# Kernel optimization log

Hardware: AMD Instinct MI355X
Metric: run time of the kernel (lower is better)

Reference implementation:

```python
import jax, jax.numpy as jnp
import numpy as np

N_HEAD = 16

def setup_inputs() -> dict:
    key = jax.random.key(0)
    ks = jax.random.split(key, 9)
    B, T, C = 4, 2048, 1024
    s = 0.02
    return {
        "x": jax.random.normal(ks[0], (B, T, C), dtype=jnp.float32),
        "Wq": jax.random.normal(ks[1], (C, C), dtype=jnp.float32) * s,
        "bq": jnp.zeros((C,), dtype=jnp.float32),
        "Wk": jax.random.normal(ks[2], (C, C), dtype=jnp.float32) * s,
        "bk": jnp.zeros((C,), dtype=jnp.float32),
        "Wv": jax.random.normal(ks[3], (C, C), dtype=jnp.float32) * s,
        "bv": jnp.zeros((C,), dtype=jnp.float32),
        "Wo": jax.random.normal(ks[4], (C, C), dtype=jnp.float32) * s,
        "bo": jnp.zeros((C,), dtype=jnp.float32),
    }

def reference(x, Wq, bq, Wk, bk, Wv, bv, Wo, bo):
    B, T, C = x.shape
    H = N_HEAD
    d = C // H
    # QKV projections (Linear: y = x @ W + b), split heads -> [B, H, T, d]
    def proj(W, b):
        return (x @ W + b).reshape(B, T, H, d).transpose(0, 2, 1, 3)
    q = proj(Wq, bq)
    k = proj(Wk, bk)
    v = proj(Wv, bv)
    scale = jnp.float32(d) ** -0.5
    scores = jnp.einsum("bhtd,bhsd->bhts", q, k) * scale  # [B,H,T,T]
    attn = jax.nn.softmax(scores, axis=-1)
    out = jnp.einsum("bhts,bhsd->bhtd", attn, v)  # [B,H,T,d]
    out = out.transpose(0, 2, 1, 3).reshape(B, T, C)
    return out @ Wo + bo
```

## Files before the change

kernel.cpp:

```cpp
#include <hip/hip_runtime.h>
#include <hip/hip_bf16.h>

typedef unsigned short u16;
typedef unsigned int   u32;

typedef __bf16 bf16x8 __attribute__((ext_vector_type(8)));
typedef float  f32x4  __attribute__((ext_vector_type(4)));

#define MFMA16(A, B, C) __builtin_amdgcn_mfma_f32_16x16x32_bf16(A, B, C, 0, 0, 0)

static __device__ __forceinline__ u16 f2bf(float f) {
  union { float f; u32 u; } v; v.f = f;
  u32 r = v.u + 0x7fffu + ((v.u >> 16) & 1u);
  return (u16)(r >> 16);
}

static __device__ __forceinline__ float exp2a(float x) {
  float r; asm("v_exp_f32 %0, %1" : "=v"(r) : "v"(x)); return r;
}
static __device__ __forceinline__ float max3f(float a, float b, float c) {
  float r; asm("v_max3_f32 %0, %1, %2, %3" : "=v"(r) : "v"(a), "v"(b), "v"(c)); return r;
}
static __device__ __forceinline__ u32 cvtpk(float lo, float hi) {
  u32 r; asm("v_cvt_pk_bf16_f32 %0, %1, %2" : "=v"(r) : "v"(lo), "v"(hi)); return r;
}

static __device__ __forceinline__ void async16(const void* g, void* l) {
  __builtin_amdgcn_global_load_lds((const __attribute__((address_space(1))) void*)g,
                                   (__attribute__((address_space(3))) void*)l, 16, 0, 0);
}

static __device__ __forceinline__ int permrow(int r) {
  return (r & 3) | (((r >> 3) & 1) << 2);
}

__global__ __launch_bounds__(256) void cvtx_k(const float* __restrict__ x, u16* __restrict__ xb) {
  size_t i = ((size_t)blockIdx.x * 256 + threadIdx.x) * 4;
  float4 v = *(const float4*)(x + i);
  u32 lo = (u32)f2bf(v.x) | ((u32)f2bf(v.y) << 16);
  u32 hi = (u32)f2bf(v.z) | ((u32)f2bf(v.w) << 16);
  *(uint2*)(xb + i) = make_uint2(lo, hi);
}

__global__ __launch_bounds__(256) void wt_k(const float* __restrict__ Wq, const float* __restrict__ Wk,
                                            const float* __restrict__ Wv, const float* __restrict__ Wo,
                                            u16* __restrict__ WT) {
  const int z = blockIdx.z;
  const float* W = (z == 0) ? Wq : (z == 1) ? Wk : (z == 2) ? Wv : Wo;
  u16* out = WT + (size_t)z * 1048576;
  __shared__ float tile[32][33];
  const int tx = threadIdx.x & 31, ty = threadIdx.x >> 5;
  const int n0 = blockIdx.x * 32, k0 = blockIdx.y * 32;
#pragma unroll
  for (int i = 0; i < 4; i++)
    tile[ty + i * 8][tx] = W[(size_t)(k0 + ty + i * 8) * 1024 + n0 + tx];
  __syncthreads();
#pragma unroll
  for (int i = 0; i < 4; i++)
    out[(size_t)(n0 + ty + i * 8) * 1024 + k0 + tx] = f2bf(tile[tx][ty + i * 8]);
}

#define G_STAGE(NXT)                                                          \
  {                                                                           \
    async16(pgA0, &As[(NXT) * 16384 + (0 * 512 + tid) * 8]);                  \
    async16(pgA1, &As[(NXT) * 16384 + (1 * 512 + tid) * 8]);                  \
    async16(pgA2, &As[(NXT) * 16384 + (2 * 512 + tid) * 8]);                  \
    async16(pgA3, &As[(NXT) * 16384 + (3 * 512 + tid) * 8]);                  \
    async16(pgB0, &Bs[(NXT) * 8192 + (0 * 512 + tid) * 8]);                   \
    async16(pgB1, &Bs[(NXT) * 8192 + (1 * 512 + tid) * 8]);                   \
    pgA0 += 64; pgA1 += 64; pgA2 += 64; pgA3 += 64; pgB0 += 64; pgB1 += 64;   \
  }

#define COMPUTE_T(CUR)                                                        \
  _Pragma("unroll")                                                           \
  for (int kk = 0; kk < 2; ++kk) {                                            \
    const u16* pAk = kk ? pA1 : pA0;                                          \
    const u16* pBk = kk ? pB1 : pB0;                                          \
    bf16x8 a0 = *(const bf16x8*)(pAk + (CUR) * 16384);                        \
    bf16x8 a1 = *(const bf16x8*)(pAk + (CUR) * 16384 + 1024);                 \
    bf16x8 a2 = *(const bf16x8*)(pAk + (CUR) * 16384 + 2048);                 \
    bf16x8 a3 = *(const bf16x8*)(pAk + (CUR) * 16384 + 3072);                 \
    bf16x8 b0 = *(const bf16x8*)(pBk + (CUR) * 8192);                         \
    bf16x8 b1 = *(const bf16x8*)(pBk + (CUR) * 8192 + 1024);                  \
    bf16x8 b2 = *(const bf16x8*)(pBk + (CUR) * 8192 + 2048);                  \
    bf16x8 b3 = *(const bf16x8*)(pBk + (CUR) * 8192 + 3072);                  \
    __builtin_amdgcn_s_setprio(1);                                            \
    acc[0][0] = MFMA16(a0, b0, acc[0][0]); acc[0][1] = MFMA16(a0, b1, acc[0][1]); \
    acc[0][2] = MFMA16(a0, b2, acc[0][2]); acc[0][3] = MFMA16(a0, b3, acc[0][3]); \
    acc[1][0] = MFMA16(a1, b0, acc[1][0]); acc[1][1] = MFMA16(a1, b1, acc[1][1]); \
    acc[1][2] = MFMA16(a1, b2, acc[1][2]); acc[1][3] = MFMA16(a1, b3, acc[1][3]); \
    acc[2][0] = MFMA16(a2, b0, acc[2][0]); acc[2][1] = MFMA16(a2, b1, acc[2][1]); \
    acc[2][2] = MFMA16(a2, b2, acc[2][2]); acc[2][3] = MFMA16(a2, b3, acc[2][3]); \
    acc[3][0] = MFMA16(a3, b0, acc[3][0]); acc[3][1] = MFMA16(a3, b1, acc[3][1]); \
    acc[3][2] = MFMA16(a3, b2, acc[3][2]); acc[3][3] = MFMA16(a3, b3, acc[3][3]); \
    __builtin_amdgcn_s_setprio(0);                                            \
  }

#define GITER(CUR, WN, STG, NXT)                                              \
  {                                                                           \
    asm volatile("s_waitcnt vmcnt(" #WN ")" ::: "memory");                    \
    __builtin_amdgcn_s_barrier();                                             \
    __builtin_amdgcn_sched_barrier(0);                                        \
    if (STG) G_STAGE(NXT)                                                     \
    COMPUTE_T(CUR)                                                            \
  }

template <int MODE>
__global__ __launch_bounds__(512, 2) void gemm256_k(const u16* __restrict__ A, const u16* __restrict__ WTall,
                                                    const float* __restrict__ b0, const float* __restrict__ b1,
                                                    const float* __restrict__ b2,
                                                    u16* __restrict__ outb, float* __restrict__ outf) {
  __shared__ u16 As[3 * 16384];
  __shared__ u16 Bs[3 * 8192];
  const int tid = threadIdx.x;
  const int lane = tid & 63;
  const int wid = tid >> 6;
  const int wm = wid >> 1, wn = wid & 1;
  const int g = lane >> 4, cc = lane & 15;

  const int bid = blockIdx.x;
  const int xcd = bid & 7;
  const int idx = bid >> 3;
  const int m0 = (xcd * 4 + (idx & 3)) * 256;
  const int nb = (idx >> 2) * 128;
  const u16* Bg = WTall + (size_t)(MODE == 0 ? 0 : 3145728) + (size_t)nb * 1024;

  const u16* pgA0; const u16* pgA1; const u16* pgA2; const u16* pgA3;
  const u16* pgB0; const u16* pgB1;
  {
    const int u0 = tid, u1 = 512 + tid, u2 = 1024 + tid, u3 = 1536 + tid;
    pgA0 = A + (size_t)(m0 + (u0 >> 3)) * 1024 + (((u0 & 7) ^ ((u0 >> 3) & 7)) << 3);
    pgA1 = A + (size_t)(m0 + (u1 >> 3)) * 1024 + (((u1 & 7) ^ ((u1 >> 3) & 7)) << 3);
    pgA2 = A + (size_t)(m0 + (u2 >> 3)) * 1024 + (((u2 & 7) ^ ((u2 >> 3) & 7)) << 3);
    pgA3 = A + (size_t)(m0 + (u3 >> 3)) * 1024 + (((u3 & 7) ^ ((u3 >> 3) & 7)) << 3);
    pgB0 = Bg + (size_t)(u0 >> 3) * 1024 + (((u0 & 7) ^ ((u0 >> 3) & 7)) << 3);
    pgB1 = Bg + (size_t)(u1 >> 3) * 1024 + (((u1 & 7) ^ ((u1 >> 3) & 7)) << 3);
  }

  const int s0 = g ^ (cc & 7);
  const u16* pA0 = As + (wm * 64 + cc) * 64 + (s0 << 3);
  const u16* pA1 = As + (wm * 64 + cc) * 64 + ((s0 ^ 4) << 3);
  const u16* pB0 = Bs + (wn * 64 + cc) * 64 + (s0 << 3);
  const u16* pB1 = Bs + (wn * 64 + cc) * 64 + ((s0 ^ 4) << 3);

  f32x4 acc[4][4] = {};

  G_STAGE(0)
  G_STAGE(1)

  for (int to = 0; to < 12; to += 3) {
    GITER(0, 6, 1, 2)
    GITER(1, 6, 1, 0)
    GITER(2, 6, 1, 1)
  }
  GITER(0, 6, 1, 2)
  GITER(1, 6, 1, 0)
  GITER(2, 6, 0, 0)
  GITER(0, 0, 0, 0)

  const int z = (MODE == 0) ? (nb >> 10) : 0;
  const float* bias = (MODE == 0) ? (z == 0 ? b0 : (z == 1 ? b1 : b2)) : b0;
  const float scl = (MODE == 0 && z == 0) ? 0.18033688011112042f : 1.0f;

#pragma unroll
  for (int mi = 0; mi < 4; mi++) {
#pragma unroll
    for (int ni = 0; ni < 4; ni++) {
      const int ng = nb + wn * 64 + ni * 16 + cc;
      const int n = (MODE == 0) ? (ng & 1023) : ng;
      const float bn = bias[n];
      const int mb = m0 + wm * 64 + mi * 16 + g * 4;
      if (MODE == 0) {
        u16* o = outb + (size_t)z * 8388608;
        if (z == 2) {
          u16 h[4];
#pragma unroll
          for (int r = 0; r < 4; r++) h[r] = f2bf(acc[mi][ni][r] + bn);
          const size_t idx2 = ((size_t)(((mb >> 11) * 16 + (n >> 6)) * 64 + (n & 63))) * 2048 + (mb & 2047);
          *(uint2*)&o[idx2] = make_uint2((u32)h[0] | ((u32)h[1] << 16), (u32)h[2] | ((u32)h[3] << 16));
        } else {
#pragma unroll
          for (int r = 0; r < 4; r++) {
            const int m = mb + r;
            const float val = (acc[mi][ni][r] + bn) * scl;
            o[((size_t)((m >> 11) * 16 + (n >> 6)) * 2048 + (m & 2047)) * 64 + (n & 63)] = f2bf(val);
          }
        }
      } else {
#pragma unroll
        for (int r = 0; r < 4; r++)
          outf[(size_t)(mb + r) * 1024 + n] = acc[mi][ni][r] + bn;
      }
    }
  }
}

#define SMAX(S0, S1, M, O, PF)                                                \
  {                                                                           \
    float pm_ = max3f(max3f(S0[0], S0[1], S0[2]),                             \
                      max3f(S0[3], S1[0], S1[1]), fmaxf(S1[2], S1[3]));       \
    if (__builtin_expect(!__all(pm_ <= M + 8.0f), 0)) {                       \
      pm_ = fmaxf(pm_, __shfl_xor(pm_, 16));                                  \
      pm_ = fmaxf(pm_, __shfl_xor(pm_, 32));                                  \
      const float mn_ = fmaxf(M, pm_);                                        \
      const float al_ = exp2a(M - mn_);                                       \
      _Pragma("unroll")                                                       \
      for (int r_ = 0; r_ < 4; ++r_) {                                        \
        const float ar_ = __shfl(al_, g * 4 + r_);                            \
        _Pragma("unroll")                                                     \
        for (int t_ = 0; t_ < 5; ++t_) O[t_][r_] *= ar_;                      \
      }                                                                       \
      M = mn_;                                                                \
    }                                                                         \
    const float e0_ = exp2a(S0[0] - M), e1_ = exp2a(S0[1] - M);               \
    const float e2_ = exp2a(S0[2] - M), e3_ = exp2a(S0[3] - M);               \
    const float e4_ = exp2a(S1[0] - M), e5_ = exp2a(S1[1] - M);               \
    const float e6_ = exp2a(S1[2] - M), e7_ = exp2a(S1[3] - M);               \
    union { u32 u[4]; bf16x8 v; } pu_;                                        \
    pu_.u[0] = cvtpk(e0_, e1_); pu_.u[1] = cvtpk(e2_, e3_);                   \
    pu_.u[2] = cvtpk(e4_, e5_); pu_.u[3] = cvtpk(e6_, e7_);                   \
    PF = pu_.v;                                                               \
  }

#define COMPUTE(BUF)                                                          \
  _Pragma("unroll")                                                           \
  for (int sub = 0; sub < 2; ++sub) {                                         \
    const u16* pV_ = sub ? pV1 : pV0;                                         \
    bf16x8 k00 = *(const bf16x8*)(pK0 + (BUF)*4096 + sub*2048);               \
    bf16x8 k01 = *(const bf16x8*)(pK1 + (BUF)*4096 + sub*2048);               \
    bf16x8 k10 = *(const bf16x8*)(pK0 + (BUF)*4096 + sub*2048 + 256);         \
    bf16x8 k11 = *(const bf16x8*)(pK1 + (BUF)*4096 + sub*2048 + 256);         \
    __builtin_amdgcn_s_setprio(1);                                            \
    f32x4 sA0 = {}, sA1 = {}, sB0 = {}, sB1 = {};                             \
    sA0 = MFMA16(k00, qfA[0], sA0); sA0 = MFMA16(k01, qfA[1], sA0);           \
    sB0 = MFMA16(k00, qfB[0], sB0); sB0 = MFMA16(k01, qfB[1], sB0);           \
    sA1 = MFMA16(k10, qfA[0], sA1); sA1 = MFMA16(k11, qfA[1], sA1);           \
    sB1 = MFMA16(k10, qfB[0], sB1); sB1 = MFMA16(k11, qfB[1], sB1);           \
    __builtin_amdgcn_s_setprio(0);                                            \
    bf16x8 pfA, pfB;                                                          \
    SMAX(sA0, sA1, mA, oA, pfA);                                              \
    SMAX(sB0, sB1, mB, oB, pfB);                                              \
    __builtin_amdgcn_s_setprio(1);                                            \
    _Pragma("unroll")                                                         \
    for (int t = 0; t < 4; ++t) {                                             \
      bf16x8 vf = *(const bf16x8*)(pV_ + (BUF)*4096 + t*1024);                \
      oA[t] = MFMA16(pfA, vf, oA[t]);                                         \
      oB[t] = MFMA16(pfB, vf, oB[t]);                                         \
    }                                                                         \
    oA[4] = MFMA16(pfA, vone, oA[4]);                                         \
    oB[4] = MFMA16(pfB, vone, oB[4]);                                         \
    __builtin_amdgcn_s_setprio(0);                                            \
  }

#define STEP(BUF, IT)                                                         \
  {                                                                           \
    __syncthreads();                                                          \
    if ((IT) < 31) {                                                          \
      const size_t ko_ = (size_t)((IT) + 1) * 4096;                           \
      const size_t vo_ = (size_t)((IT) + 1) * 64;                             \
      async16(kS0 + ko_, &Ks[((BUF) ^ 1) * 4096 + tid * 8]);                  \
      async16(kS1 + ko_, &Ks[((BUF) ^ 1) * 4096 + tid * 8 + 2048]);           \
      async16(vS0 + vo_, &Vs[((BUF) ^ 1) * 4096 + tid * 8]);                  \
      async16(vS1 + vo_, &Vs[((BUF) ^ 1) * 4096 + tid * 8 + 2048]);           \
    }                                                                         \
    COMPUTE(BUF)                                                              \
  }

__global__ __launch_bounds__(256, 4) void attn_k(const u16* __restrict__ Qg, const u16* __restrict__ Kg,
                                                 const u16* __restrict__ Vtg, u16* __restrict__ ctx) {
  __shared__ u16 Ks[8192];
  __shared__ u16 Vs[8192];
  const int tid = threadIdx.x;
  const int lane = tid & 63;
  const int wid = tid >> 6;
  const int g = lane >> 4, cc = lane & 15;
  const int a_ = cc >> 2, b_ = cc & 3;

  const int bid = blockIdx.x;
  const int xcd = bid & 7, tt = bid >> 3;
  const int bh = xcd * 8 + (tt >> 4);
  const int q0 = (tt & 15) * 128 + wid * 16;
  const size_t base = (size_t)bh * 131072;

  bf16x8 qfA[2], qfB[2];
#pragma unroll
  for (int c2 = 0; c2 < 2; c2++) {
    qfA[c2] = *(const bf16x8*)(Qg + base + (size_t)(q0 + cc) * 64 + c2 * 32 + g * 8);
    qfB[c2] = *(const bf16x8*)(Qg + base + (size_t)(q0 + 64 + cc) * 64 + c2 * 32 + g * 8);
  }

  bf16x8 vone;
#pragma unroll
  for (int j = 0; j < 8; j++) vone[j] = (__bf16)1.0f;

  float mA = -30000.0f, mB = -30000.0f;
  f32x4 oA[5] = {}, oB[5] = {};

  const int cK = b_ | ((a_ & 1) << 2);
  const int slK = g ^ cK;
  const u16* pK0 = &Ks[(8 * a_ + b_) * 64 + (slK << 3)];
  const u16* pK1 = &Ks[(8 * a_ + b_) * 64 + ((slK ^ 4) << 3)];
  const int cV = b_ | (((cc >> 3) & 1) << 2);
  const u16* pV0 = &Vs[cc * 64 + ((g ^ cV) << 3)];
  const u16* pV1 = &Vs[cc * 64 + (((4 + g) ^ cV) << 3)];

  const int r0 = tid >> 3, r1 = r0 + 32;
  const int slot = tid & 7;
  const int sp0 = slot ^ permrow(r0), sp1 = slot ^ permrow(r1);
  const u16* kS0 = Kg + base + (size_t)r0 * 64 + (sp0 << 3);
  const u16* kS1 = Kg + base + (size_t)r1 * 64 + (sp1 << 3);
  const u16* vS0 = Vtg + base + (size_t)r0 * 2048 + (sp0 << 3);
  const u16* vS1 = Vtg + base + (size_t)r1 * 2048 + (sp1 << 3);

  async16(kS0, &Ks[tid * 8]);
  async16(kS1, &Ks[tid * 8 + 2048]);
  async16(vS0, &Vs[tid * 8]);
  async16(vS1, &Vs[tid * 8 + 2048]);

  for (int it = 0; it < 32; it += 2) {
    STEP(0, it)
    STEP(1, it + 1)
  }

  const int b = bh >> 4, h = bh & 15;
#pragma unroll
  for (int r = 0; r < 4; r++) {
    {
      const float inv = __builtin_amdgcn_rcpf(oA[4][r]);
      const int q = q0 + g * 4 + r;
#pragma unroll
      for (int t = 0; t < 4; t++)
        ctx[((size_t)((b * 2048 + q) * 16 + h)) * 64 + t * 16 + cc] = f2bf(oA[t][r] * inv);
    }
    {
      const float inv = __builtin_amdgcn_rcpf(oB[4][r]);
      const int q = q0 + 64 + g * 4 + r;
#pragma unroll
      for (int t = 0; t < 4; t++)
        ctx[((size_t)((b * 2048 + q) * 16 + h)) * 64 + t * 16 + cc] = f2bf(oB[t][r] * inv);
    }
  }
}

extern "C" void kernel_launch(void* const* d_in, const int* in_sizes, int n_in,
                              void* d_out, int out_size, void* d_ws, size_t ws_size,
                              hipStream_t stream) {
  const float* x  = (const float*)d_in[0];
  const float* Wq = (const float*)d_in[1];
  const float* bq = (const float*)d_in[2];
  const float* Wk = (const float*)d_in[3];
  const float* bk = (const float*)d_in[4];
  const float* Wv = (const float*)d_in[5];
  const float* bv = (const float*)d_in[6];
  const float* Wo = (const float*)d_in[7];
  const float* bo = (const float*)d_in[8];
  float* out = (float*)d_out;

  char* w = (char*)d_ws;
  u16* xb   = (u16*)(w);
  u16* WT   = (u16*)(w + (16u << 20));
  u16* QKV  = (u16*)(w + (24u << 20));
  u16* ctxb = (u16*)(w + (72u << 20));

  cvtx_k<<<dim3(8192), dim3(256), 0, stream>>>(x, xb);
  wt_k<<<dim3(32, 32, 4), dim3(256), 0, stream>>>(Wq, Wk, Wv, Wo, WT);
  gemm256_k<0><<<dim3(768), dim3(512), 0, stream>>>(xb, WT, bq, bk, bv, QKV, nullptr);
  attn_k<<<dim3(1024), dim3(256), 0, stream>>>(QKV, QKV + 8388608, QKV + 2 * 8388608, ctxb);
  gemm256_k<1><<<dim3(256), dim3(512), 0, stream>>>(ctxb, WT, bo, nullptr, nullptr, nullptr, out);
}
```

Before: 179.0 us.

## Restructure projection GEMM to 4 waves with 64x128 warp tiles and BK=32

The GEMM kernel drops from 8 waves of 512 threads to 4 waves of 256 threads. Each wave now computes a 64x128 tile (4x8 MFMA accumulators) over a 256x128 block tile. The K step is halved to 32 with a 3-stage async pipeline of 32 iterations, and the LDS swizzle is adjusted to match. The larger per-wave tile raises MFMA reuse of each LDS fragment and cuts LDS traffic per flop. The cost is more accumulator registers, less latency hiding from fewer waves, and twice as many barriers.

```diff
diff --git a/kernel.cpp b/kernel.cpp
--- a/kernel.cpp
+++ b/kernel.cpp
@@ -60,62 +60,70 @@
     out[(size_t)(n0 + ty + i * 8) * 1024 + k0 + tx] = f2bf(tile[tx][ty + i * 8]);
 }
 
-#define G_STAGE(NXT)                                                          \
-  {                                                                           \
-    async16(pgA0, &As[(NXT) * 16384 + (0 * 512 + tid) * 8]);                  \
-    async16(pgA1, &As[(NXT) * 16384 + (1 * 512 + tid) * 8]);                  \
-    async16(pgA2, &As[(NXT) * 16384 + (2 * 512 + tid) * 8]);                  \
-    async16(pgA3, &As[(NXT) * 16384 + (3 * 512 + tid) * 8]);                  \
-    async16(pgB0, &Bs[(NXT) * 8192 + (0 * 512 + tid) * 8]);                   \
-    async16(pgB1, &Bs[(NXT) * 8192 + (1 * 512 + tid) * 8]);                   \
-    pgA0 += 64; pgA1 += 64; pgA2 += 64; pgA3 += 64; pgB0 += 64; pgB1 += 64;   \
-  }
-
-#define COMPUTE_T(CUR)                                                        \
-  _Pragma("unroll")                                                           \
-  for (int kk = 0; kk < 2; ++kk) {                                            \
-    const u16* pAk = kk ? pA1 : pA0;                                          \
-    const u16* pBk = kk ? pB1 : pB0;                                          \
-    bf16x8 a0 = *(const bf16x8*)(pAk + (CUR) * 16384);                        \
-    bf16x8 a1 = *(const bf16x8*)(pAk + (CUR) * 16384 + 1024);                 \
-    bf16x8 a2 = *(const bf16x8*)(pAk + (CUR) * 16384 + 2048);                 \
-    bf16x8 a3 = *(const bf16x8*)(pAk + (CUR) * 16384 + 3072);                 \
-    bf16x8 b0 = *(const bf16x8*)(pBk + (CUR) * 8192);                         \
-    bf16x8 b1 = *(const bf16x8*)(pBk + (CUR) * 8192 + 1024);                  \
-    bf16x8 b2 = *(const bf16x8*)(pBk + (CUR) * 8192 + 2048);                  \
-    bf16x8 b3 = *(const bf16x8*)(pBk + (CUR) * 8192 + 3072);                  \
+#define G2_STAGE(NXT)                                                         \
+  {                                                                           \
+    async16(pa0, &As2[(NXT) * 8192 + tid * 8]);                               \
+    async16(pa1, &As2[(NXT) * 8192 + (256 + tid) * 8]);                       \
+    async16(pa2, &As2[(NXT) * 8192 + (512 + tid) * 8]);                       \
+    async16(pa3, &As2[(NXT) * 8192 + (768 + tid) * 8]);                       \
+    async16(pb0, &Bs2[(NXT) * 4096 + tid * 8]);                               \
+    async16(pb1, &Bs2[(NXT) * 4096 + (256 + tid) * 8]);                       \
+    pa0 += 32; pa1 += 32; pa2 += 32; pa3 += 32; pb0 += 32; pb1 += 32;         \
+  }
+
+#define COMPUTE2(CUR)                                                         \
+  {                                                                           \
+    bf16x8 a0 = *(const bf16x8*)(pA + (CUR) * 8192);                          \
+    bf16x8 a1 = *(const bf16x8*)(pA + (CUR) * 8192 + 512);                    \
+    bf16x8 a2 = *(const bf16x8*)(pA + (CUR) * 8192 + 1024);                   \
+    bf16x8 a3 = *(const bf16x8*)(pA + (CUR) * 8192 + 1536);                   \
+    bf16x8 b0 = *(const bf16x8*)(pB + (CUR) * 4096);                          \
+    bf16x8 b1 = *(const bf16x8*)(pB + (CUR) * 4096 + 512);                    \
+    bf16x8 b2 = *(const bf16x8*)(pB + (CUR) * 4096 + 1024);                   \
+    bf16x8 b3 = *(const bf16x8*)(pB + (CUR) * 4096 + 1536);                   \
+    bf16x8 b4 = *(const bf16x8*)(pB + (CUR) * 4096 + 2048);                   \
+    bf16x8 b5 = *(const bf16x8*)(pB + (CUR) * 4096 + 2560);                   \
+    bf16x8 b6 = *(const bf16x8*)(pB + (CUR) * 4096 + 3072);                   \
+    bf16x8 b7 = *(const bf16x8*)(pB + (CUR) * 4096 + 3584);                   \
     __builtin_amdgcn_s_setprio(1);                                            \
     acc[0][0] = MFMA16(a0, b0, acc[0][0]); acc[0][1] = MFMA16(a0, b1, acc[0][1]); \
     acc[0][2] = MFMA16(a0, b2, acc[0][2]); acc[0][3] = MFMA16(a0, b3, acc[0][3]); \
+    acc[0][4] = MFMA16(a0, b4, acc[0][4]); acc[0][5] = MFMA16(a0, b5, acc[0][5]); \
+    acc[0][6] = MFMA16(a0, b6, acc[0][6]); acc[0][7] = MFMA16(a0, b7, acc[0][7]); \
     acc[1][0] = MFMA16(a1, b0, acc[1][0]); acc[1][1] = MFMA16(a1, b1, acc[1][1]); \
     acc[1][2] = MFMA16(a1, b2, acc[1][2]); acc[1][3] = MFMA16(a1, b3, acc[1][3]); \
+    acc[1][4] = MFMA16(a1, b4, acc[1][4]); acc[1][5] = MFMA16(a1, b5, acc[1][5]); \
+    acc[1][6] = MFMA16(a1, b6, acc[1][6]); acc[1][7] = MFMA16(a1, b7, acc[1][7]); \
     acc[2][0] = MFMA16(a2, b0, acc[2][0]); acc[2][1] = MFMA16(a2, b1, acc[2][1]); \
     acc[2][2] = MFMA16(a2, b2, acc[2][2]); acc[2][3] = MFMA16(a2, b3, acc[2][3]); \
+    acc[2][4] = MFMA16(a2, b4, acc[2][4]); acc[2][5] = MFMA16(a2, b5, acc[2][5]); \
+    acc[2][6] = MFMA16(a2, b6, acc[2][6]); acc[2][7] = MFMA16(a2, b7, acc[2][7]); \
     acc[3][0] = MFMA16(a3, b0, acc[3][0]); acc[3][1] = MFMA16(a3, b1, acc[3][1]); \
     acc[3][2] = MFMA16(a3, b2, acc[3][2]); acc[3][3] = MFMA16(a3, b3, acc[3][3]); \
+    acc[3][4] = MFMA16(a3, b4, acc[3][4]); acc[3][5] = MFMA16(a3, b5, acc[3][5]); \
+    acc[3][6] = MFMA16(a3, b6, acc[3][6]); acc[3][7] = MFMA16(a3, b7, acc[3][7]); \
     __builtin_amdgcn_s_setprio(0);                                            \
   }
 
-#define GITER(CUR, WN, STG, NXT)                                              \
+#define GITER2(CUR, WN, STG, NXT)                                             \
   {                                                                           \
     asm volatile("s_waitcnt vmcnt(" #WN ")" ::: "memory");                    \
     __builtin_amdgcn_s_barrier();                                             \
     __builtin_amdgcn_sched_barrier(0);                                        \
-    if (STG) G_STAGE(NXT)                                                     \
-    COMPUTE_T(CUR)                                                            \
+    if (STG) G2_STAGE(NXT)                                                    \
+    COMPUTE2(CUR)                                                             \
   }
 
 template <int MODE>
-__global__ __launch_bounds__(512, 2) void gemm256_k(const u16* __restrict__ A, const u16* __restrict__ WTall,
+__global__ __launch_bounds__(256, 2) void gemm256_k(const u16* __restrict__ A, const u16* __restrict__ WTall,
                                                     const float* __restrict__ b0, const float* __restrict__ b1,
                                                     const float* __restrict__ b2,
                                                     u16* __restrict__ outb, float* __restrict__ outf) {
-  __shared__ u16 As[3 * 16384];
-  __shared__ u16 Bs[3 * 8192];
+  __shared__ u16 As2[3 * 8192];
+  __shared__ u16 Bs2[3 * 4096];
   const int tid = threadIdx.x;
   const int lane = tid & 63;
   const int wid = tid >> 6;
-  const int wm = wid >> 1, wn = wid & 1;
   const int g = lane >> 4, cc = lane & 15;
 
   const int bid = blockIdx.x;
@@ -125,38 +133,34 @@
   const int nb = (idx >> 2) * 128;
   const u16* Bg = WTall + (size_t)(MODE == 0 ? 0 : 3145728) + (size_t)nb * 1024;
 
-  const u16* pgA0; const u16* pgA1; const u16* pgA2; const u16* pgA3;
-  const u16* pgB0; const u16* pgB1;
+  const u16* pa0; const u16* pa1; const u16* pa2; const u16* pa3;
+  const u16* pb0; const u16* pb1;
   {
-    const int u0 = tid, u1 = 512 + tid, u2 = 1024 + tid, u3 = 1536 + tid;
-    pgA0 = A + (size_t)(m0 + (u0 >> 3)) * 1024 + (((u0 & 7) ^ ((u0 >> 3) & 7)) << 3);
-    pgA1 = A + (size_t)(m0 + (u1 >> 3)) * 1024 + (((u1 & 7) ^ ((u1 >> 3) & 7)) << 3);
-    pgA2 = A + (size_t)(m0 + (u2 >> 3)) * 1024 + (((u2 & 7) ^ ((u2 >> 3) & 7)) << 3);
-    pgA3 = A + (size_t)(m0 + (u3 >> 3)) * 1024 + (((u3 & 7) ^ ((u3 >> 3) & 7)) << 3);
-    pgB0 = Bg + (size_t)(u0 >> 3) * 1024 + (((u0 & 7) ^ ((u0 >> 3) & 7)) << 3);
-    pgB1 = Bg + (size_t)(u1 >> 3) * 1024 + (((u1 & 7) ^ ((u1 >> 3) & 7)) << 3);
-  }
-
-  const int s0 = g ^ (cc & 7);
-  const u16* pA0 = As + (wm * 64 + cc) * 64 + (s0 << 3);
-  const u16* pA1 = As + (wm * 64 + cc) * 64 + ((s0 ^ 4) << 3);
-  const u16* pB0 = Bs + (wn * 64 + cc) * 64 + (s0 << 3);
-  const u16* pB1 = Bs + (wn * 64 + cc) * 64 + ((s0 ^ 4) << 3);
-
-  f32x4 acc[4][4] = {};
-
-  G_STAGE(0)
-  G_STAGE(1)
-
-  for (int to = 0; to < 12; to += 3) {
-    GITER(0, 6, 1, 2)
-    GITER(1, 6, 1, 0)
-    GITER(2, 6, 1, 1)
-  }
-  GITER(0, 6, 1, 2)
-  GITER(1, 6, 1, 0)
-  GITER(2, 6, 0, 0)
-  GITER(0, 0, 0, 0)
+    const int u0 = tid, u1 = 256 + tid, u2 = 512 + tid, u3 = 768 + tid;
+    pa0 = A + (size_t)(m0 + (u0 >> 2)) * 1024 + (((u0 & 3) ^ ((u0 >> 2) & 3)) << 3);
+    pa1 = A + (size_t)(m0 + (u1 >> 2)) * 1024 + (((u1 & 3) ^ ((u1 >> 2) & 3)) << 3);
+    pa2 = A + (size_t)(m0 + (u2 >> 2)) * 1024 + (((u2 & 3) ^ ((u2 >> 2) & 3)) << 3);
+    pa3 = A + (size_t)(m0 + (u3 >> 2)) * 1024 + (((u3 & 3) ^ ((u3 >> 2) & 3)) << 3);
+    pb0 = Bg + (size_t)(u0 >> 2) * 1024 + (((u0 & 3) ^ ((u0 >> 2) & 3)) << 3);
+    pb1 = Bg + (size_t)(u1 >> 2) * 1024 + (((u1 & 3) ^ ((u1 >> 2) & 3)) << 3);
+  }
+
+  const int sw = g ^ (cc & 3);
+  const u16* pA = As2 + (wid * 64 + cc) * 32 + (sw << 3);
+  const u16* pB = Bs2 + cc * 32 + (sw << 3);
+
+  f32x4 acc[4][8] = {};
+
+  G2_STAGE(0)
+  G2_STAGE(1)
+
+  for (int to = 0; to < 30; to += 3) {
+    GITER2(0, 6, 1, 2)
+    GITER2(1, 6, 1, 0)
+    GITER2(2, 6, 1, 1)
+  }
+  GITER2(0, 6, 0, 0)
+  GITER2(1, 0, 0, 0)
 
   const int z = (MODE == 0) ? (nb >> 10) : 0;
   const float* bias = (MODE == 0) ? (z == 0 ? b0 : (z == 1 ? b1 : b2)) : b0;
@@ -165,19 +169,19 @@
 #pragma unroll
   for (int mi = 0; mi < 4; mi++) {
 #pragma unroll
-    for (int ni = 0; ni < 4; ni++) {
-      const int ng = nb + wn * 64 + ni * 16 + cc;
+    for (int ni = 0; ni < 8; ni++) {
+      const int ng = nb + ni * 16 + cc;
       const int n = (MODE == 0) ? (ng & 1023) : ng;
       const float bn = bias[n];
-      const int mb = m0 + wm * 64 + mi * 16 + g * 4;
+      const int mb = m0 + wid * 64 + mi * 16 + g * 4;
       if (MODE == 0) {
         u16* o = outb + (size_t)z * 8388608;
         if (z == 2) {
           u16 h[4];
 #pragma unroll
           for (int r = 0; r < 4; r++) h[r] = f2bf(acc[mi][ni][r] + bn);
-          const size_t idx2 = ((size_t)(((mb >> 11) * 16 + (n >> 6)) * 64 + (n & 63))) * 2048 + (mb & 2047);
-          *(uint2*)&o[idx2] = make_uint2((u32)h[0] | ((u32)h[1] << 16), (u32)h[2] | ((u32)h[3] << 16));
+          const size_t ix = ((size_t)(((mb >> 11) * 16 + (n >> 6)) * 64 + (n & 63))) * 2048 + (mb & 2047);
+          *(uint2*)&o[ix] = make_uint2((u32)h[0] | ((u32)h[1] << 16), (u32)h[2] | ((u32)h[3] << 16));
         } else {
 #pragma unroll
           for (int r = 0; r < 4; r++) {
@@ -364,7 +368,7 @@
 
   cvtx_k<<<dim3(8192), dim3(256), 0, stream>>>(x, xb);
   wt_k<<<dim3(32, 32, 4), dim3(256), 0, stream>>>(Wq, Wk, Wv, Wo, WT);
-  gemm256_k<0><<<dim3(768), dim3(512), 0, stream>>>(xb, WT, bq, bk, bv, QKV, nullptr);
+  gemm256_k<0><<<dim3(768), dim3(256), 0, stream>>>(xb, WT, bq, bk, bv, QKV, nullptr);
   attn_k<<<dim3(1024), dim3(256), 0, stream>>>(QKV, QKV + 8388608, QKV + 2 * 8388608, ctxb);
-  gemm256_k<1><<<dim3(256), dim3(512), 0, stream>>>(ctxb, WT, bo, nullptr, nullptr, nullptr, out);
-}
+  gemm256_k<1><<<dim3(256), dim3(256), 0, stream>>>(ctxb, WT, bo, nullptr, nullptr, nullptr, out);
+}
```

New measurement: 193.0 us. +7.8%, slower.
